# Kernel optimization log

Hardware: AMD Instinct MI355X
Metric: run time of the kernel (lower is better)

Reference implementation:

```python
import jax, jax.numpy as jnp
import numpy as np
import math

FLAT_DIM = 30_000_000
SIZE = 1 << 25  # 33_554_432, next pow2 >= FLAT_DIM


def fwht(x):
    """Iterative fast Walsh-Hadamard transform, same butterfly ordering as the torch code."""
    size = x.shape[0]
    h = 1
    while h < size:
        x = x.reshape(-1, 2 * h)
        left, right = x[:, :h], x[:, h:]
        x = jnp.concatenate([left + right, left - right], axis=1)
        h *= 2
    return x.reshape(size)


def setup_inputs() -> dict:
    key = jax.random.key(0)
    k1, k2, k3, k4 = jax.random.split(key, 4)
    theta = jax.random.normal(k1, (FLAT_DIM,), dtype=jnp.float32)
    G = jax.random.normal(k2, (SIZE,), dtype=jnp.float32)
    B = (jax.random.randint(k3, (SIZE,), 0, 2) * 2 - 1).astype(jnp.float32)
    Pi = jax.random.permutation(k4, SIZE)
    divisor = jnp.sqrt(SIZE * jnp.sum(G * G))  # scalar, computed from G as in __init__
    return {"theta": theta, "G": G, "B": B, "divisor": divisor, "Pi": Pi}


def reference(theta, G, B, divisor, Pi):
    flat_dim = theta.shape[0]
    size = G.shape[0]
    theta_padded = jnp.pad(theta, (0, size - flat_dim)) * B
    hbx = fwht(theta_padded)
    pihbx = hbx[Pi]
    gpihbx = pihbx * G
    hgpihbx = fwht(gpihbx)
    result = hgpihbx[:flat_dim]
    scale = divisor * jnp.sqrt(jnp.float32(flat_dim) / jnp.float32(size))
    return result / scale
```

## Files before the change

### kernel.cpp

```cpp
#include <hip/hip_runtime.h>
#include <math.h>

#define SIZE_N   (1 << 25)
#define FLATD    30000000
#define FLATD4   7500000
#define LOW_N    8192
#define HIGH_N   4096

__global__ __launch_bounds__(512) void k1_padB_fwht_low(const float* __restrict__ theta,
                                                        const float* __restrict__ B,
                                                        float* __restrict__ x) {
    __shared__ float lds[LOW_N];
    float4* lds4 = (float4*)lds;
    const int t   = threadIdx.x;
    const int blk = blockIdx.x;
    const int base4 = blk * (LOW_N / 4);
    const float4* B4  = (const float4*)B;
    const float4* th4 = (const float4*)theta;

#pragma unroll
    for (int i = 0; i < 4; ++i) {
        int l4 = t + (i << 9);
        int g4 = base4 + l4;
        float4 b = B4[g4];
        float4 v = make_float4(0.f, 0.f, 0.f, 0.f);
        if (g4 < FLATD4) v = th4[g4];
        v.x *= b.x; v.y *= b.y; v.z *= b.z; v.w *= b.w;
        lds4[l4] = v;
    }

    for (int s = 0; s < 13; ++s) {
        __syncthreads();
        int h = 1 << s;
#pragma unroll
        for (int i = 0; i < 8; ++i) {
            int p   = t + (i << 9);
            int idx = ((p >> s) << (s + 1)) | (p & (h - 1));
            float a = lds[idx];
            float b2 = lds[idx + h];
            lds[idx]     = a + b2;
            lds[idx + h] = a - b2;
        }
    }
    __syncthreads();

    float4* x4 = (float4*)x;
#pragma unroll
    for (int i = 0; i < 4; ++i) {
        int l4 = t + (i << 9);
        x4[base4 + l4] = lds4[l4];
    }
}

__global__ __launch_bounds__(512) void k2_fwht_high(float* __restrict__ x) {
    __shared__ float lds[HIGH_N * 4];
    float4* lds4 = (float4*)lds;
    const int t   = threadIdx.x;
    const int hw  = blockIdx.x;
    const int blk = ((hw & 7) << 8) | (hw >> 3);
    float4* x4 = (float4*)x;

#pragma unroll
    for (int i = 0; i < 8; ++i) {
        int r = t + (i << 9);
        lds4[r] = x4[r * 2048 + blk];
    }

    for (int s = 0; s < 12; ++s) {
        __syncthreads();
        int h = 1 << s;
#pragma unroll
        for (int i = 0; i < 16; ++i) {
            int w = t + (i << 9);
            int c = w & 3;
            int p = w >> 2;
            int r = ((p >> s) << (s + 1)) | (p & (h - 1));
            int a0 = (r << 2) | c;
            int a1 = ((r + h) << 2) | c;
            float a = lds[a0];
            float b = lds[a1];
            lds[a0] = a + b;
            lds[a1] = a - b;
        }
    }
    __syncthreads();

#pragma unroll
    for (int i = 0; i < 8; ++i) {
        int r = t + (i << 9);
        x4[r * 2048 + blk] = lds4[r];
    }
}

__global__ __launch_bounds__(512) void k3_gather_fwht_low(const float* __restrict__ x,
                                                          const int* __restrict__ Pi,
                                                          const float* __restrict__ G,
                                                          float* __restrict__ y) {
    __shared__ float lds[LOW_N];
    float4* lds4 = (float4*)lds;
    const int t   = threadIdx.x;
    const int blk = blockIdx.x;
    const int base4 = blk * (LOW_N / 4);
    const int4*   Pi4 = (const int4*)Pi;
    const float4* G4  = (const float4*)G;

#pragma unroll
    for (int i = 0; i < 4; ++i) {
        int l4 = t + (i << 9);
        int g4 = base4 + l4;
        int4   p4 = Pi4[g4];
        float4 g  = G4[g4];
        float4 v;
        v.x = x[p4.x] * g.x;
        v.y = x[p4.y] * g.y;
        v.z = x[p4.z] * g.z;
        v.w = x[p4.w] * g.w;
        lds4[l4] = v;
    }

    for (int s = 0; s < 13; ++s) {
        __syncthreads();
        int h = 1 << s;
#pragma unroll
        for (int i = 0; i < 8; ++i) {
            int p   = t + (i << 9);
            int idx = ((p >> s) << (s + 1)) | (p & (h - 1));
            float a = lds[idx];
            float b2 = lds[idx + h];
            lds[idx]     = a + b2;
            lds[idx + h] = a - b2;
        }
    }
    __syncthreads();

    float4* y4 = (float4*)y;
#pragma unroll
    for (int i = 0; i < 4; ++i) {
        int l4 = t + (i << 9);
        y4[base4 + l4] = lds4[l4];
    }
}

__global__ __launch_bounds__(512) void k4_fwht_high_out(const float* __restrict__ y,
                                                        const float* __restrict__ divisor,
                                                        float* __restrict__ out) {
    __shared__ float lds[HIGH_N * 4];
    float4* lds4 = (float4*)lds;
    const int t   = threadIdx.x;
    const int hw  = blockIdx.x;
    const int blk = ((hw & 7) << 8) | (hw >> 3);
    const float4* y4 = (const float4*)y;

#pragma unroll
    for (int i = 0; i < 8; ++i) {
        int r = t + (i << 9);
        lds4[r] = y4[r * 2048 + blk];
    }

    const float scale = divisor[0] * sqrtf((float)FLATD / (float)SIZE_N);
    const float inv   = 1.0f / scale;

    for (int s = 0; s < 12; ++s) {
        __syncthreads();
        int h = 1 << s;
#pragma unroll
        for (int i = 0; i < 16; ++i) {
            int w = t + (i << 9);
            int c = w & 3;
            int p = w >> 2;
            int r = ((p >> s) << (s + 1)) | (p & (h - 1));
            int a0 = (r << 2) | c;
            int a1 = ((r + h) << 2) | c;
            float a = lds[a0];
            float b = lds[a1];
            lds[a0] = a + b;
            lds[a1] = a - b;
        }
    }
    __syncthreads();

    float4* out4 = (float4*)out;
#pragma unroll
    for (int i = 0; i < 8; ++i) {
        int r  = t + (i << 9);
        int o4 = r * 2048 + blk;
        if (o4 < FLATD4) {
            float4 v = lds4[r];
            v.x *= inv; v.y *= inv; v.z *= inv; v.w *= inv;
            out4[o4] = v;
        }
    }
}

extern "C" void kernel_launch(void* const* d_in, const int* in_sizes, int n_in,
                              void* d_out, int out_size, void* d_ws, size_t ws_size,
                              hipStream_t stream) {
    const float* theta   = (const float*)d_in[0];
    const float* G       = (const float*)d_in[1];
    const float* B       = (const float*)d_in[2];
    const float* divisor = (const float*)d_in[3];
    const int*   Pi      = (const int*)d_in[4];
    float* out = (float*)d_out;

    float* x = (float*)d_ws;
    float* y = x + SIZE_N;

    k1_padB_fwht_low<<<SIZE_N / LOW_N, 512, 0, stream>>>(theta, B, x);
    k2_fwht_high<<<LOW_N / 4, 512, 0, stream>>>(x);
    k3_gather_fwht_low<<<SIZE_N / LOW_N, 512, 0, stream>>>(x, Pi, G, y);
    k4_fwht_high_out<<<LOW_N / 4, 512, 0, stream>>>(y, divisor, out);
}
```

Measured before the change: 1.365 ms.

## Split 12-stage high FWHT into two 6-stage passes with contiguous row tiles

Replaces each 12-stage high-stride FWHT kernel with two 6-stage kernels. Each block loads 64 rows of 256 contiguous floats at stride 2048 or 131072 float4s, instead of single float4 columns at a 2048-float4 stride. This is meant to improve global memory coalescing and halve LDS butterfly work per pass by using float4 butterflies. The cost is an extra full read and write pass over the 128 MB buffer for each transform.

```diff
diff --git a/kernel.cpp b/kernel.cpp
--- a/kernel.cpp
+++ b/kernel.cpp
@@ -5,7 +5,6 @@
 #define FLATD    30000000
 #define FLATD4   7500000
 #define LOW_N    8192
-#define HIGH_N   4096
 
 __global__ __launch_bounds__(512) void k1_padB_fwht_low(const float* __restrict__ theta,
                                                         const float* __restrict__ B,
@@ -52,43 +51,102 @@
     }
 }
 
-__global__ __launch_bounds__(512) void k2_fwht_high(float* __restrict__ x) {
-    __shared__ float lds[HIGH_N * 4];
-    float4* lds4 = (float4*)lds;
-    const int t   = threadIdx.x;
-    const int hw  = blockIdx.x;
-    const int blk = ((hw & 7) << 8) | (hw >> 3);
+__global__ __launch_bounds__(512) void k_high6(float* __restrict__ x, int A4, int R4) {
+    __shared__ float lds[64 * 256];
+    float4* lds4 = (float4*)lds;
+    const int t   = threadIdx.x;
+    const int blk = blockIdx.x;
+    const int base4 = (blk >> 5) * A4 + (blk & 31) * 64;
     float4* x4 = (float4*)x;
 
 #pragma unroll
     for (int i = 0; i < 8; ++i) {
-        int r = t + (i << 9);
-        lds4[r] = x4[r * 2048 + blk];
-    }
-
-    for (int s = 0; s < 12; ++s) {
-        __syncthreads();
-        int h = 1 << s;
-#pragma unroll
-        for (int i = 0; i < 16; ++i) {
-            int w = t + (i << 9);
-            int c = w & 3;
-            int p = w >> 2;
-            int r = ((p >> s) << (s + 1)) | (p & (h - 1));
-            int a0 = (r << 2) | c;
-            int a1 = ((r + h) << 2) | c;
-            float a = lds[a0];
-            float b = lds[a1];
-            lds[a0] = a + b;
-            lds[a1] = a - b;
-        }
-    }
-    __syncthreads();
-
-#pragma unroll
-    for (int i = 0; i < 8; ++i) {
-        int r = t + (i << 9);
-        x4[r * 2048 + blk] = lds4[r];
+        int idx = t + (i << 9);
+        int row = idx >> 6;
+        int l4  = idx & 63;
+        lds4[idx] = x4[base4 + row * R4 + l4];
+    }
+
+    for (int s = 0; s < 6; ++s) {
+        __syncthreads();
+        int h = 1 << s;
+#pragma unroll
+        for (int i = 0; i < 4; ++i) {
+            int w  = t + (i << 9);
+            int p  = w >> 6;
+            int l4 = w & 63;
+            int r0 = ((p >> s) << (s + 1)) | (p & (h - 1));
+            int a0 = (r0 << 6) | l4;
+            int a1 = ((r0 + h) << 6) | l4;
+            float4 a = lds4[a0];
+            float4 b = lds4[a1];
+            lds4[a0] = make_float4(a.x + b.x, a.y + b.y, a.z + b.z, a.w + b.w);
+            lds4[a1] = make_float4(a.x - b.x, a.y - b.y, a.z - b.z, a.w - b.w);
+        }
+    }
+    __syncthreads();
+
+#pragma unroll
+    for (int i = 0; i < 8; ++i) {
+        int idx = t + (i << 9);
+        int row = idx >> 6;
+        int l4  = idx & 63;
+        x4[base4 + row * R4 + l4] = lds4[idx];
+    }
+}
+
+__global__ __launch_bounds__(512) void k_high6_out(const float* __restrict__ y,
+                                                   const float* __restrict__ divisor,
+                                                   float* __restrict__ out) {
+    __shared__ float lds[64 * 256];
+    float4* lds4 = (float4*)lds;
+    const int t   = threadIdx.x;
+    const int blk = blockIdx.x;
+    const int base4 = (blk >> 5) * 2048 + (blk & 31) * 64;
+    const float4* y4 = (const float4*)y;
+
+#pragma unroll
+    for (int i = 0; i < 8; ++i) {
+        int idx = t + (i << 9);
+        int row = idx >> 6;
+        int l4  = idx & 63;
+        lds4[idx] = y4[base4 + row * 131072 + l4];
+    }
+
+    const float scale = divisor[0] * sqrtf((float)FLATD / (float)SIZE_N);
+    const float inv   = 1.0f / scale;
+
+    for (int s = 0; s < 6; ++s) {
+        __syncthreads();
+        int h = 1 << s;
+#pragma unroll
+        for (int i = 0; i < 4; ++i) {
+            int w  = t + (i << 9);
+            int p  = w >> 6;
+            int l4 = w & 63;
+            int r0 = ((p >> s) << (s + 1)) | (p & (h - 1));
+            int a0 = (r0 << 6) | l4;
+            int a1 = ((r0 + h) << 6) | l4;
+            float4 a = lds4[a0];
+            float4 b = lds4[a1];
+            lds4[a0] = make_float4(a.x + b.x, a.y + b.y, a.z + b.z, a.w + b.w);
+            lds4[a1] = make_float4(a.x - b.x, a.y - b.y, a.z - b.z, a.w - b.w);
+        }
+    }
+    __syncthreads();
+
+    float4* out4 = (float4*)out;
+#pragma unroll
+    for (int i = 0; i < 8; ++i) {
+        int idx = t + (i << 9);
+        int row = idx >> 6;
+        int l4  = idx & 63;
+        int o4  = base4 + row * 131072 + l4;
+        if (o4 < FLATD4) {
+            float4 v = lds4[idx];
+            v.x *= inv; v.y *= inv; v.z *= inv; v.w *= inv;
+            out4[o4] = v;
+        }
     }
 }
 
@@ -141,57 +199,6 @@
     }
 }
 
-__global__ __launch_bounds__(512) void k4_fwht_high_out(const float* __restrict__ y,
-                                                        const float* __restrict__ divisor,
-                                                        float* __restrict__ out) {
-    __shared__ float lds[HIGH_N * 4];
-    float4* lds4 = (float4*)lds;
-    const int t   = threadIdx.x;
-    const int hw  = blockIdx.x;
-    const int blk = ((hw & 7) << 8) | (hw >> 3);
-    const float4* y4 = (const float4*)y;
-
-#pragma unroll
-    for (int i = 0; i < 8; ++i) {
-        int r = t + (i << 9);
-        lds4[r] = y4[r * 2048 + blk];
-    }
-
-    const float scale = divisor[0] * sqrtf((float)FLATD / (float)SIZE_N);
-    const float inv   = 1.0f / scale;
-
-    for (int s = 0; s < 12; ++s) {
-        __syncthreads();
-        int h = 1 << s;
-#pragma unroll
-        for (int i = 0; i < 16; ++i) {
-            int w = t + (i << 9);
-            int c = w & 3;
-            int p = w >> 2;
-            int r = ((p >> s) << (s + 1)) | (p & (h - 1));
-            int a0 = (r << 2) | c;
-            int a1 = ((r + h) << 2) | c;
-            float a = lds[a0];
-            float b = lds[a1];
-            lds[a0] = a + b;
-            lds[a1] = a - b;
-        }
-    }
-    __syncthreads();
-
-    float4* out4 = (float4*)out;
-#pragma unroll
-    for (int i = 0; i < 8; ++i) {
-        int r  = t + (i << 9);
-        int o4 = r * 2048 + blk;
-        if (o4 < FLATD4) {
-            float4 v = lds4[r];
-            v.x *= inv; v.y *= inv; v.z *= inv; v.w *= inv;
-            out4[o4] = v;
-        }
-    }
-}
-
 extern "C" void kernel_launch(void* const* d_in, const int* in_sizes, int n_in,
                               void* d_out, int out_size, void* d_ws, size_t ws_size,
                               hipStream_t stream) {
@@ -206,7 +213,9 @@
     float* y = x + SIZE_N;
 
     k1_padB_fwht_low<<<SIZE_N / LOW_N, 512, 0, stream>>>(theta, B, x);
-    k2_fwht_high<<<LOW_N / 4, 512, 0, stream>>>(x);
+    k_high6<<<2048, 512, 0, stream>>>(x, 131072, 2048);
+    k_high6<<<2048, 512, 0, stream>>>(x, 2048, 131072);
     k3_gather_fwht_low<<<SIZE_N / LOW_N, 512, 0, stream>>>(x, Pi, G, y);
-    k4_fwht_high_out<<<LOW_N / 4, 512, 0, stream>>>(y, divisor, out);
-}
+    k_high6<<<2048, 512, 0, stream>>>(y, 131072, 2048);
+    k_high6_out<<<2048, 512, 0, stream>>>(y, divisor, out);
+}
```

Result: faster. 1.306 ms (-4.3%).
